# Kernel optimization log

Measured on AMD Instinct MI355X. Metric: run time of the kernel, lower is better.

Reference implementation:

```python
import jax, jax.numpy as jnp
import numpy as np

N, E = 50000, 800000
F_NODE, F_EDGE, H, LAT, MAXN = 128, 16, 128, 64, 200


def setup_inputs() -> dict:
    key = jax.random.key(0)
    ks = jax.random.split(key, 40)
    s = 0.05
    p = {
        'x': jax.random.normal(ks[0], (N, F_NODE), jnp.float32),
        'edge_index': jax.random.randint(ks[1], (2, E), 0, N, jnp.int64),
        'edge_attr': jax.random.normal(ks[2], (E, F_EDGE), jnp.float32),
        'eps': jax.random.normal(ks[3], (1, LAT), jnp.float32),
        'num_nodes': N,
        # GATConv layer 1 (heads=1)
        'W1': jax.random.normal(ks[4], (F_NODE, H), jnp.float32) * s,
        'att_src1': jax.random.normal(ks[5], (H,), jnp.float32) * s,
        'att_dst1': jax.random.normal(ks[6], (H,), jnp.float32) * s,
        'We1': jax.random.normal(ks[7], (F_EDGE, H), jnp.float32) * s,
        'att_e1': jax.random.normal(ks[8], (H,), jnp.float32) * s,
        'b1': jnp.zeros((H,), jnp.float32),
        # GATConv layer 2
        'W2': jax.random.normal(ks[9], (H, H), jnp.float32) * s,
        'att_src2': jax.random.normal(ks[10], (H,), jnp.float32) * s,
        'att_dst2': jax.random.normal(ks[11], (H,), jnp.float32) * s,
        'We2': jax.random.normal(ks[12], (F_EDGE, H), jnp.float32) * s,
        'att_e2': jax.random.normal(ks[13], (H,), jnp.float32) * s,
        'b2': jnp.zeros((H,), jnp.float32),
        # heads
        'mu_W': jax.random.normal(ks[14], (H, LAT), jnp.float32) * s,
        'mu_b': jnp.zeros((LAT,), jnp.float32),
        'lv_W': jax.random.normal(ks[15], (H, LAT), jnp.float32) * s,
        'lv_b': jnp.zeros((LAT,), jnp.float32),
        'dec_W': jax.random.normal(ks[16], (LAT, H), jnp.float32) * s,
        'dec_b': jnp.zeros((H,), jnp.float32),
        'adj_W1': jax.random.normal(ks[17], (H, H), jnp.float32) * s,
        'adj_b1': jnp.zeros((H,), jnp.float32),
        'adj_W2': jax.random.normal(ks[18], (H, MAXN), jnp.float32) * s,
        'adj_b2': jnp.zeros((MAXN,), jnp.float32),
        'nd_W1': jax.random.normal(ks[19], (H, H), jnp.float32) * s,
        'nd_b1': jnp.zeros((H,), jnp.float32),
        'nd_W2': jax.random.normal(ks[20], (H, F_NODE), jnp.float32) * s,
        'nd_b2': jnp.zeros((F_NODE,), jnp.float32),
    }
    return p


def _gat(h, src, dst, ea, W, a_s, a_d, We, a_e, b, n):
    # PyG GATConv, heads=1: linear transform, per-edge attention, segment softmax over dst
    g = h @ W                                     # [n, H]
    alpha = jax.nn.leaky_relu((g @ a_s)[src] + (g @ a_d)[dst] + (ea @ We) @ a_e,
                              negative_slope=0.2)  # [E']
    m = jax.ops.segment_max(alpha, dst, num_segments=n)
    ex = jnp.exp(alpha - m[dst])
    den = jax.ops.segment_sum(ex, dst, num_segments=n)
    w = ex / den[dst]
    return jax.ops.segment_sum(w[:, None] * g[src], dst, num_segments=n) + b


def _forward(x, edge_index, edge_attr, eps, num_nodes,
             W1, att_src1, att_dst1, We1, att_e1, b1,
             W2, att_src2, att_dst2, We2, att_e2, b2,
             mu_W, mu_b, lv_W, lv_b, dec_W, dec_b,
             adj_W1, adj_b1, adj_W2, adj_b2, nd_W1, nd_b1, nd_W2, nd_b2):
    n = x.shape[0]
    src, dst = edge_index[0], edge_index[1]
    # add self loops; self-loop edge_attr = per-node mean of incoming edge_attr (PyG fill_value='mean')
    deg = jax.ops.segment_sum(jnp.ones((src.shape[0],), x.dtype), dst, num_segments=n)
    mean_ea = jax.ops.segment_sum(edge_attr, dst, num_segments=n) / jnp.maximum(deg, 1.0)[:, None]
    loop = jnp.arange(n)
    src_f = jnp.concatenate([src, loop])
    dst_f = jnp.concatenate([dst, loop])
    ea_f = jnp.concatenate([edge_attr, mean_ea])
    h = jax.nn.relu(_gat(x, src_f, dst_f, ea_f, W1, att_src1, att_dst1, We1, att_e1, b1, n))
    h = jax.nn.relu(_gat(h, src_f, dst_f, ea_f, W2, att_src2, att_dst2, We2, att_e2, b2, n))
    hg = h.mean(axis=0, keepdims=True)            # global_mean_pool, single graph -> [1, H]
    mu = hg @ mu_W + mu_b
    logvar = hg @ lv_W + lv_b
    z = mu + eps * jnp.exp(0.5 * logvar)
    hd = jax.nn.relu(z @ dec_W + dec_b)           # [1, H]
    hn = jnp.broadcast_to(hd[:, None, :], (1, num_nodes, hd.shape[-1]))
    adj = jax.nn.relu(hn @ adj_W1 + adj_b1) @ adj_W2 + adj_b2   # [1, n, MAXN]
    adj = adj[:, :, :num_nodes]
    nodes = jax.nn.relu(hn @ nd_W1 + nd_b1) @ nd_W2 + nd_b2     # [1, n, F_NODE]
    return adj, nodes, mu, logvar


def reference(x, edge_index, edge_attr, eps, num_nodes,
              W1, att_src1, att_dst1, We1, att_e1, b1,
              W2, att_src2, att_dst2, We2, att_e2, b2,
              mu_W, mu_b, lv_W, lv_b, dec_W, dec_b,
              adj_W1, adj_b1, adj_W2, adj_b2, nd_W1, nd_b1, nd_W2, nd_b2):
    return _forward(x, edge_index, edge_attr, eps, num_nodes,
                    W1, att_src1, att_dst1, We1, att_e1, b1,
                    W2, att_src2, att_dst2, We2, att_e2, b2,
                    mu_W, mu_b, lv_W, lv_b, dec_W, dec_b,
                    adj_W1, adj_b1, adj_W2, adj_b2, nd_W1, nd_b1, nd_W2, nd_b2)
```

## Files before the change

kernel.cpp:

```cpp
#include <hip/hip_runtime.h>
#include <math.h>

#define NN   50000
#define EE   800000
#define EF   850000
#define HH   128
#define FE   16
#define LATD 64
#define MAXNN 200

#define ADJ_TOT   10000000
#define NODES_TOT 6400000
#define OUT_TOT   16400000
#define MU_OFF    16400000
#define LV_OFF    16400064

typedef __attribute__((ext_vector_type(8))) short bf16x8;
typedef __attribute__((ext_vector_type(4))) float f32x4;
typedef __attribute__((ext_vector_type(2))) float f32x2;

__device__ __forceinline__ unsigned short f2bf(float f){
  unsigned int u = __float_as_uint(f);
  unsigned int r = (u + 0x7FFFu + ((u>>16)&1u)) >> 16;
  return (unsigned short)r;
}
__device__ __forceinline__ float bf2f(unsigned short h){
  return __uint_as_float(((unsigned int)h)<<16);
}

__global__ void ksetup(int* ideg, float* hgsum,
                       const float* We1, const float* ae1, const float* We2, const float* ae2,
                       float* wa1, float* wa2,
                       const float* W1, const float* W2,
                       unsigned short* Wp1, unsigned short* Wp2){
  int i = blockIdx.x*blockDim.x + threadIdx.x;
  if(i < NN) ideg[i]=0;
  if(i < HH) hgsum[i]=0.f;
  if(i < FE){
    float s1=0.f, s2=0.f;
    for(int j=0;j<HH;j++){ s1 += We1[i*HH+j]*ae1[j]; s2 += We2[i*HH+j]*ae2[j]; }
    wa1[i]=s1; wa2[i]=s2;
  }
  if(i < HH*HH){
    int n = i >> 7, k = i & 127;
    Wp1[i] = f2bf(W1[k*HH + n]);
    Wp2[i] = f2bf(W2[k*HH + n]);
  }
}

__global__ void kdeg(const int* __restrict__ ei, int* ideg, unsigned short* __restrict__ erank){
  int e = blockIdx.x*blockDim.x + threadIdx.x;
  if(e<EE) erank[e] = (unsigned short)atomicAdd(&ideg[ei[EE+e]], 1);
}

__global__ void kscan1(const int* __restrict__ ideg, int* rowstart, int* blocksum){
  __shared__ int sd[1024];
  int t=threadIdx.x; int i=blockIdx.x*1024+t;
  int v = (i<NN)? (ideg[i]+1) : 0;
  sd[t]=v; __syncthreads();
  for(int off=1; off<1024; off<<=1){
    int x = (t>=off)? sd[t-off] : 0;
    __syncthreads();
    sd[t] += x;
    __syncthreads();
  }
  if(i<NN) rowstart[i] = sd[t]-v;
  if(t==1023) blocksum[blockIdx.x]=sd[1023];
}
__global__ void kscan2(const int* blocksum, int* blockoff, int nb){
  if(threadIdx.x==0){
    int run=0;
    for(int b=0;b<nb;b++){ blockoff[b]=run; run+=blocksum[b]; }
    blockoff[nb]=run;
  }
}
__global__ void kscan3(int* rowstart, const int* __restrict__ blockoff, int nb){
  int i=blockIdx.x*blockDim.x+threadIdx.x;
  if(i<NN) rowstart[i]+=blockoff[i>>10];
  if(i==0) rowstart[NN]=blockoff[nb];
}

__global__ void kscatter(const int* __restrict__ ei, const float* __restrict__ ea,
                         const float* __restrict__ wa1, const float* __restrict__ wa2,
                         const int* __restrict__ rowstart, const unsigned short* __restrict__ erank,
                         uint2* __restrict__ csr){
  int e=blockIdx.x*blockDim.x+threadIdx.x;
  if(e>=EE) return;
  int s=ei[e], d=ei[EE+e];
  const float4* ea4 = (const float4*)(ea + (size_t)e*FE);
  float4 v0=ea4[0], v1=ea4[1], v2=ea4[2], v3=ea4[3];
  float va[16]={v0.x,v0.y,v0.z,v0.w, v1.x,v1.y,v1.z,v1.w,
                v2.x,v2.y,v2.z,v2.w, v3.x,v3.y,v3.z,v3.w};
  float d1=0.f,d2=0.f;
  #pragma unroll
  for(int f=0;f<FE;f++){ d1+=va[f]*wa1[f]; d2+=va[f]*wa2[f]; }
  int pos = rowstart[d] + (int)erank[e];
  uint2 en; en.x = (unsigned)s;
  en.y = (unsigned)f2bf(d1) | ((unsigned)f2bf(d2)<<16);
  csr[pos] = en;
}

__global__ __launch_bounds__(256) void kself(const int* __restrict__ rowstart,
                      const int* __restrict__ ideg,
                      uint2* __restrict__ csr){
  int tid = threadIdx.x;
  int l16 = tid & 15;
  int grp = tid >> 4;
  int i = blockIdx.x*16 + grp;
  if(i>=NN) return;
  int base = rowstart[i]; int deg = ideg[i];
  float s1=0.f, s2=0.f;
  for(int k=l16;k<deg;k+=16){
    uint2 en=csr[base+k];
    s1 += bf2f((unsigned short)(en.y & 0xFFFFu));
    s2 += bf2f((unsigned short)(en.y >> 16));
  }
  #pragma unroll
  for(int m=8;m>=1;m>>=1){ s1+=__shfl_xor(s1,m,16); s2+=__shfl_xor(s2,m,16); }
  if(l16==0){
    float dg = (float)deg; if(dg<1.f) dg=1.f;
    uint2 en; en.x=(unsigned)i;
    en.y = (unsigned)f2bf(s1/dg) | ((unsigned)f2bf(s2/dg)<<16);
    csr[base+deg] = en;
  }
}

__global__ __launch_bounds__(256) void kgemm3(const void* __restrict__ hin, int h_is_fp32,
    const unsigned short* __restrict__ Wp,
    const float* __restrict__ atts, const float* __restrict__ attd,
    unsigned char* __restrict__ A8, float* __restrict__ asrc, float* __restrict__ adst){
  int lane = threadIdx.x & 63;
  int wid  = threadIdx.x >> 6;
  int l = lane & 15, q = lane >> 4;
  int r0 = blockIdx.x*64 + wid*16;
  if(r0 >= NN) return;
  const unsigned short* hb = (const unsigned short*)hin;
  const float*          hf = (const float*)hin;
  int row = r0 + l;

  f32x4 acc[8];
  #pragma unroll
  for(int t=0;t<8;t++) acc[t]=(f32x4){0.f,0.f,0.f,0.f};

  #pragma unroll
  for(int kb=0;kb<4;kb++){
    bf16x8 a;
    if(h_is_fp32){
      const float* p = hf + (size_t)row*HH + kb*32 + q*8;
      float4 u0 = *(const float4*)(p);
      float4 u1 = *(const float4*)(p+4);
      a[0]=(short)f2bf(u0.x); a[1]=(short)f2bf(u0.y); a[2]=(short)f2bf(u0.z); a[3]=(short)f2bf(u0.w);
      a[4]=(short)f2bf(u1.x); a[5]=(short)f2bf(u1.y); a[6]=(short)f2bf(u1.z); a[7]=(short)f2bf(u1.w);
    } else {
      a = *(const bf16x8*)(hb + (size_t)row*HH + kb*32 + q*8);
    }
    #pragma unroll
    for(int t=0;t<8;t++){
      bf16x8 b = *(const bf16x8*)(Wp + (size_t)(t*16+l)*HH + kb*32 + q*8);
      acc[t] = __builtin_amdgcn_mfma_f32_16x16x32_bf16(a, b, acc[t], 0,0,0);
    }
  }

  float av[8], dv[8];
  #pragma unroll
  for(int t=0;t<8;t++){ av[t]=atts[t*16+l]; dv[t]=attd[t*16+l]; }
  #pragma unroll
  for(int reg=0;reg<4;reg++){
    float ps=0.f, pd=0.f;
    #pragma unroll
    for(int t=0;t<8;t++){ ps+=acc[t][reg]*av[t]; pd+=acc[t][reg]*dv[t]; }
    #pragma unroll
    for(int m=8;m>=1;m>>=1){ ps+=__shfl_xor(ps,m,16); pd+=__shfl_xor(pd,m,16); }
    if(l==0){ int R=r0+q*4+reg; asrc[R]=ps; adst[R]=pd; }
  }
  #pragma unroll
  for(int t=0;t<8;t++)
    #pragma unroll
    for(int reg=0;reg<4;reg++){
      int pk = __builtin_amdgcn_cvt_pk_fp8_f32(acc[t][reg], 0.f, 0, false);
      A8[(size_t)(r0+q*4+reg)*HH + t*16 + l] = (unsigned char)(pk & 0xFF);
    }
}

__global__ __launch_bounds__(256) void kgat(const unsigned char* __restrict__ A8,
    const float* __restrict__ asrc, const float* __restrict__ adst,
    const int* __restrict__ rowstart, const uint2* __restrict__ csr,
    int etsel, const float* __restrict__ bias,
    float* __restrict__ alphabuf, int* __restrict__ srcbuf,
    unsigned short* __restrict__ Bout){
  int lane = threadIdx.x & 63;
  int wid  = threadIdx.x >> 6;
  int i = blockIdx.x*4 + wid;
  if(i >= NN) return;
  int base = rowstart[i]; int len = rowstart[i+1]-base;
  int lq = lane >> 3;
  int lf = lane & 7;
  float adi = adst[i];
  float den;
  float av[16];
  #pragma unroll
  for(int j=0;j<16;j++) av[j]=0.f;

  if(__builtin_expect(len <= 64, 1)){
    float a = -1e30f; int s=0;
    if(lane < len){
      uint2 en = csr[base+lane];
      s = (int)en.x;
      float et = etsel ? bf2f((unsigned short)(en.y>>16)) : bf2f((unsigned short)(en.y&0xFFFFu));
      a = asrc[s] + adi + et;
      a = a>0.f ? a : 0.2f*a;
    }
    float m = a;
    #pragma unroll
    for(int mk=32;mk>=1;mk>>=1) m = fmaxf(m, __shfl_xor(m, mk));
    float ex = (lane<len) ? __expf(a-m) : 0.f;
    float sm = ex;
    #pragma unroll
    for(int mk=32;mk>=1;mk>>=1) sm += __shfl_xor(sm, mk);
    den = sm;
    int chunks = (len+7)>>3;
    float wk = __shfl(ex, lq);
    int   sk = __shfl(s, lq);
    uint4 p  = *((const uint4*)(A8 + (size_t)sk*HH) + lf);
    for(int c=0;c<chunks;c++){
      float wc = wk; uint4 pc = p;
      if(c+1<chunks){
        int idx = (c+1)*8 + lq;
        wk = __shfl(ex, idx);
        sk = __shfl(s, idx);
        p  = *((const uint4*)(A8 + (size_t)sk*HH) + lf);
      }
      f32x2 v;
      v=__builtin_amdgcn_cvt_pk_f32_fp8(pc.x,false); av[0]+=wc*v[0];  av[1]+=wc*v[1];
      v=__builtin_amdgcn_cvt_pk_f32_fp8(pc.x,true ); av[2]+=wc*v[0];  av[3]+=wc*v[1];
      v=__builtin_amdgcn_cvt_pk_f32_fp8(pc.y,false); av[4]+=wc*v[0];  av[5]+=wc*v[1];
      v=__builtin_amdgcn_cvt_pk_f32_fp8(pc.y,true ); av[6]+=wc*v[0];  av[7]+=wc*v[1];
      v=__builtin_amdgcn_cvt_pk_f32_fp8(pc.z,false); av[8]+=wc*v[0];  av[9]+=wc*v[1];
      v=__builtin_amdgcn_cvt_pk_f32_fp8(pc.z,true ); av[10]+=wc*v[0]; av[11]+=wc*v[1];
      v=__builtin_amdgcn_cvt_pk_f32_fp8(pc.w,false); av[12]+=wc*v[0]; av[13]+=wc*v[1];
      v=__builtin_amdgcn_cvt_pk_f32_fp8(pc.w,true ); av[14]+=wc*v[0]; av[15]+=wc*v[1];
    }
  } else {
    float lm = -1e30f;
    for(int k=lane;k<len;k+=64){
      uint2 en = csr[base+k];
      int s = (int)en.x;
      float et = etsel ? bf2f((unsigned short)(en.y>>16)) : bf2f((unsigned short)(en.y&0xFFFFu));
      float a = asrc[s] + adi + et;
      a = a>0.f ? a : 0.2f*a;
      alphabuf[base+k]=a; srcbuf[base+k]=s;
      lm = fmaxf(lm,a);
    }
    #pragma unroll
    for(int mk=32;mk>=1;mk>>=1) lm = fmaxf(lm, __shfl_xor(lm, mk));
    float ls=0.f;
    for(int k=lane;k<len;k+=64){
      float ex = __expf(alphabuf[base+k]-lm);
      alphabuf[base+k]=ex; ls+=ex;
    }
    #pragma unroll
    for(int mk=32;mk>=1;mk>>=1) ls += __shfl_xor(ls, mk);
    den = ls;
    int chunks = (len+7)>>3;
    for(int c=0;c<chunks;c++){
      int idx = c*8 + lq;
      float wc = (idx<len)? alphabuf[base+idx] : 0.f;
      int   sk = (idx<len)? srcbuf[base+idx] : 0;
      uint4 pc = *((const uint4*)(A8 + (size_t)sk*HH) + lf);
      f32x2 v;
      v=__builtin_amdgcn_cvt_pk_f32_fp8(pc.x,false); av[0]+=wc*v[0];  av[1]+=wc*v[1];
      v=__builtin_amdgcn_cvt_pk_f32_fp8(pc.x,true ); av[2]+=wc*v[0];  av[3]+=wc*v[1];
      v=__builtin_amdgcn_cvt_pk_f32_fp8(pc.y,false); av[4]+=wc*v[0];  av[5]+=wc*v[1];
      v=__builtin_amdgcn_cvt_pk_f32_fp8(pc.y,true ); av[6]+=wc*v[0];  av[7]+=wc*v[1];
      v=__builtin_amdgcn_cvt_pk_f32_fp8(pc.z,false); av[8]+=wc*v[0];  av[9]+=wc*v[1];
      v=__builtin_amdgcn_cvt_pk_f32_fp8(pc.z,true ); av[10]+=wc*v[0]; av[11]+=wc*v[1];
      v=__builtin_amdgcn_cvt_pk_f32_fp8(pc.w,false); av[12]+=wc*v[0]; av[13]+=wc*v[1];
      v=__builtin_amdgcn_cvt_pk_f32_fp8(pc.w,true ); av[14]+=wc*v[0]; av[15]+=wc*v[1];
    }
  }
  #pragma unroll
  for(int j=0;j<16;j++){
    av[j] += __shfl_xor(av[j],8);
    av[j] += __shfl_xor(av[j],16);
    av[j] += __shfl_xor(av[j],32);
  }
  if(lq==0){
    float inv = 1.f/den;
    const float4* bp = (const float4*)(bias + lf*16);
    float4 b0=bp[0], b1=bp[1], b2=bp[2], b3=bp[3];
    float o[16];
    o[0] =fmaxf(av[0] *inv+b0.x,0.f); o[1] =fmaxf(av[1] *inv+b0.y,0.f);
    o[2] =fmaxf(av[2] *inv+b0.z,0.f); o[3] =fmaxf(av[3] *inv+b0.w,0.f);
    o[4] =fmaxf(av[4] *inv+b1.x,0.f); o[5] =fmaxf(av[5] *inv+b1.y,0.f);
    o[6] =fmaxf(av[6] *inv+b1.z,0.f); o[7] =fmaxf(av[7] *inv+b1.w,0.f);
    o[8] =fmaxf(av[8] *inv+b2.x,0.f); o[9] =fmaxf(av[9] *inv+b2.y,0.f);
    o[10]=fmaxf(av[10]*inv+b2.z,0.f); o[11]=fmaxf(av[11]*inv+b2.w,0.f);
    o[12]=fmaxf(av[12]*inv+b3.x,0.f); o[13]=fmaxf(av[13]*inv+b3.y,0.f);
    o[14]=fmaxf(av[14]*inv+b3.z,0.f); o[15]=fmaxf(av[15]*inv+b3.w,0.f);
    uint4 ov1, ov2;
    ov1.x=(unsigned)f2bf(o[0]) |((unsigned)f2bf(o[1]) <<16);
    ov1.y=(unsigned)f2bf(o[2]) |((unsigned)f2bf(o[3]) <<16);
    ov1.z=(unsigned)f2bf(o[4]) |((unsigned)f2bf(o[5]) <<16);
    ov1.w=(unsigned)f2bf(o[6]) |((unsigned)f2bf(o[7]) <<16);
    ov2.x=(unsigned)f2bf(o[8]) |((unsigned)f2bf(o[9]) <<16);
    ov2.y=(unsigned)f2bf(o[10])|((unsigned)f2bf(o[11])<<16);
    ov2.z=(unsigned)f2bf(o[12])|((unsigned)f2bf(o[13])<<16);
    ov2.w=(unsigned)f2bf(o[14])|((unsigned)f2bf(o[15])<<16);
    uint4* outp = (uint4*)(Bout + (size_t)i*HH + lf*16);
    outp[0]=ov1; outp[1]=ov2;
  }
}

__global__ __launch_bounds__(256) void khg(const unsigned short* __restrict__ B, float* hgsum){
  int f = threadIdx.x & 127;
  int half = threadIdx.x >> 7;
  float s=0.f;
  for(int i = blockIdx.x*2+half; i < NN; i += gridDim.x*2)
    s += bf2f(B[(size_t)i*HH + f]);
  __shared__ float sd[256];
  sd[threadIdx.x]=s; __syncthreads();
  if(half==0) atomicAdd(&hgsum[f], sd[threadIdx.x]+sd[threadIdx.x+128]);
}

__global__ __launch_bounds__(256) void kdec(const float* __restrict__ hgsum, const float* __restrict__ eps,
   const float* muW,const float* mub,const float* lvW,const float* lvb,
   const float* decW,const float* decb,
   const float* aW1,const float* ab1,const float* aW2,const float* ab2,
   const float* nW1,const float* nb1,const float* nW2,const float* nb2,
   float* out, float* rowadj, float* rownodes){
  __shared__ float hg[HH], z[LATD], hd[HH], t1[HH], t2[HH];
  int t=threadIdx.x;
  if(t<HH) hg[t]=hgsum[t]*(1.0f/NN);
  __syncthreads();
  if(t<LATD){
    float mu=mub[t], lv=lvb[t];
    for(int k=0;k<HH;k++){ mu += hg[k]*muW[k*LATD+t]; lv += hg[k]*lvW[k*LATD+t]; }
    out[MU_OFF+t]=mu; out[LV_OFF+t]=lv;
    z[t]=mu + eps[t]*expf(0.5f*lv);
  }
  __syncthreads();
  if(t<HH){
    float a=decb[t];
    for(int k=0;k<LATD;k++) a += z[k]*decW[k*HH+t];
    hd[t]=fmaxf(a,0.f);
  }
  __syncthreads();
  if(t<HH){
    float a=ab1[t];
    for(int k=0;k<HH;k++) a += hd[k]*aW1[k*HH+t];
    t1[t]=fmaxf(a,0.f);
  } else {
    int j=t-HH;
    float a=nb1[j];
    for(int k=0;k<HH;k++) a += hd[k]*nW1[k*HH+j];
    t2[j]=fmaxf(a,0.f);
  }
  __syncthreads();
  for(int j=t;j<MAXNN;j+=256){
    float a=ab2[j];
    for(int k=0;k<HH;k++) a += t1[k]*aW2[k*MAXNN+j];
    rowadj[j]=a;
  }
  if(t<HH){
    float a=nb2[t];
    for(int k=0;k<HH;k++) a += t2[k]*nW2[k*HH+t];
    rownodes[t]=a;
  }
}

__global__ __launch_bounds__(256) void kbcast(const float* __restrict__ rowadj,
                                              const float* __restrict__ rownodes,
                                              float* __restrict__ out){
  __shared__ float row[MAXNN+HH];
  int t=threadIdx.x;
  if(t<MAXNN) row[t]=rowadj[t];
  if(t<HH) row[MAXNN+t]=rownodes[t];
  __syncthreads();
  int stride=gridDim.x*blockDim.x;
  for(int idx=blockIdx.x*blockDim.x+t; idx<OUT_TOT; idx+=stride){
    if(idx<ADJ_TOT) out[idx]=row[idx%MAXNN];
    else { int j=(idx-ADJ_TOT)&(HH-1); out[idx]=row[MAXNN+j]; }
  }
}

extern "C" void kernel_launch(void* const* d_in, const int* in_sizes, int n_in,
                              void* d_out, int out_size, void* d_ws, size_t ws_size,
                              hipStream_t stream){
  const float* x   = (const float*)d_in[0];
  const int*   ei  = (const int*)d_in[1];
  const float* ea  = (const float*)d_in[2];
  const float* eps = (const float*)d_in[3];
  const float* W1  =(const float*)d_in[5];
  const float* as1 =(const float*)d_in[6];
  const float* ad1 =(const float*)d_in[7];
  const float* We1 =(const float*)d_in[8];
  const float* ae1 =(const float*)d_in[9];
  const float* b1  =(const float*)d_in[10];
  const float* W2  =(const float*)d_in[11];
  const float* as2 =(const float*)d_in[12];
  const float* ad2 =(const float*)d_in[13];
  const float* We2 =(const float*)d_in[14];
  const float* ae2 =(const float*)d_in[15];
  const float* b2  =(const float*)d_in[16];
  const float* muW =(const float*)d_in[17];
  const float* mub =(const float*)d_in[18];
  const float* lvW =(const float*)d_in[19];
  const float* lvb =(const float*)d_in[20];
  const float* decW=(const float*)d_in[21];
  const float* decb=(const float*)d_in[22];
  const float* aW1 =(const float*)d_in[23];
  const float* ab1 =(const float*)d_in[24];
  const float* aW2 =(const float*)d_in[25];
  const float* ab2 =(const float*)d_in[26];
  const float* nW1 =(const float*)d_in[27];
  const float* nb1 =(const float*)d_in[28];
  const float* nW2 =(const float*)d_in[29];
  const float* nb2 =(const float*)d_in[30];
  float* out=(float*)d_out;

  char* w=(char*)d_ws;
  unsigned char*  A8  = (unsigned char*)w;  w += (size_t)NN*HH;
  unsigned short* Bbf = (unsigned short*)w; w += (size_t)NN*HH*2;
  unsigned short* Wp1 = (unsigned short*)w; w += (size_t)HH*HH*2;
  unsigned short* Wp2 = (unsigned short*)w; w += (size_t)HH*HH*2;
  uint2*  csr      = (uint2*)w;  w += (size_t)EF*8;
  float*  alphabuf = (float*)w;  w += (size_t)EF*4;
  int*    srcbuf   = (int*)w;    w += (size_t)EF*4;
  unsigned short* erank = (unsigned short*)w; w += (size_t)EE*2;
  int*    rowstart = (int*)w;    w += (size_t)(NN+1)*4;
  int*    ideg     = (int*)w;    w += (size_t)NN*4;
  float*  asrc     = (float*)w;  w += (size_t)NN*4;
  float*  adst     = (float*)w;  w += (size_t)NN*4;
  float*  hgsum    = (float*)w;  w += 128*4;
  float*  wa1      = (float*)w;  w += 16*4;
  float*  wa2      = (float*)w;  w += 16*4;
  float*  rowadj   = (float*)w;  w += 256*4;
  float*  rownodes = (float*)w;  w += 128*4;
  int*    blocksum = (int*)w;    w += 64*4;
  int*    blockoff = (int*)w;    w += 64*4;

  int nb = (NN+1023)/1024;
  int gemmblocks = (NN+63)/64;
  int gatblocks  = (NN+3)/4;

  hipLaunchKernelGGL(ksetup, dim3((NN+255)/256), dim3(256), 0, stream,
                     ideg, hgsum, We1, ae1, We2, ae2, wa1, wa2, W1, W2, Wp1, Wp2);
  hipLaunchKernelGGL(kdeg, dim3((EE+255)/256), dim3(256), 0, stream, ei, ideg, erank);
  hipLaunchKernelGGL(kscan1, dim3(nb), dim3(1024), 0, stream, ideg, rowstart, blocksum);
  hipLaunchKernelGGL(kscan2, dim3(1), dim3(64), 0, stream, blocksum, blockoff, nb);
  hipLaunchKernelGGL(kscan3, dim3((NN+255)/256), dim3(256), 0, stream, rowstart, blockoff, nb);
  hipLaunchKernelGGL(kscatter, dim3((EE+255)/256), dim3(256), 0, stream,
                     ei, ea, wa1, wa2, rowstart, erank, csr);
  hipLaunchKernelGGL(kself, dim3((NN+15)/16), dim3(256), 0, stream, rowstart, ideg, csr);
  hipLaunchKernelGGL(kgemm3, dim3(gemmblocks), dim3(256), 0, stream,
                     (const void*)x, 1, Wp1, as1, ad1, A8, asrc, adst);
  hipLaunchKernelGGL(kgat,  dim3(gatblocks), dim3(256), 0, stream, A8, asrc, adst, rowstart, csr, 0, b1, alphabuf, srcbuf, Bbf);
  hipLaunchKernelGGL(kgemm3, dim3(gemmblocks), dim3(256), 0, stream,
                     (const void*)Bbf, 0, Wp2, as2, ad2, A8, asrc, adst);
  hipLaunchKernelGGL(kgat,  dim3(gatblocks), dim3(256), 0, stream, A8, asrc, adst, rowstart, csr, 1, b2, alphabuf, srcbuf, Bbf);
  hipLaunchKernelGGL(khg,   dim3(512), dim3(256), 0, stream, Bbf, hgsum);
  hipLaunchKernelGGL(kdec,  dim3(1), dim3(256), 0, stream, hgsum, eps,
                     muW,mub,lvW,lvb,decW,decb,aW1,ab1,aW2,ab2,nW1,nb1,nW2,nb2,
                     out, rowadj, rownodes);
  hipLaunchKernelGGL(kbcast, dim3(2048), dim3(256), 0, stream, rowadj, rownodes, out);
}
```

Baseline: 441.3 us.

## Fuse setup/degree and scatter/gemm kernels, fold self-loop into GAT, vectorize broadcast

Merges the degree-count kernel with setup, replaces the zeroing with a memset, and runs scatter and the first GEMM as disjoint block ranges of one launch. The separate self-loop kernel is removed; the GAT kernel now computes the mean edge-attention of the self loop itself. The aggregation switches from 8-lane chunked uint4 loads to a per-neighbor readlane loop, with each lane handling two features and normalising up front. The single-thread kscan2 becomes a wave shuffle scan, and the broadcast writes float4. The aim is fewer launches and less work per node, at the cost of more serial per-neighbor loads in the GAT loop.

```diff
diff --git a/kernel.cpp b/kernel.cpp
--- a/kernel.cpp
+++ b/kernel.cpp
@@ -15,6 +15,9 @@
 #define MU_OFF    16400000
 #define LV_OFF    16400064
 
+#define SCATBLOCKS 3125
+#define GEMMBLOCKS 782
+
 typedef __attribute__((ext_vector_type(8))) short bf16x8;
 typedef __attribute__((ext_vector_type(4))) float f32x4;
 typedef __attribute__((ext_vector_type(2))) float f32x2;
@@ -27,15 +30,18 @@
 __device__ __forceinline__ float bf2f(unsigned short h){
   return __uint_as_float(((unsigned int)h)<<16);
 }
-
-__global__ void ksetup(int* ideg, float* hgsum,
+__device__ __forceinline__ float rlanef(float v, int k){
+  return __int_as_float(__builtin_amdgcn_readlane(__float_as_int(v), k));
+}
+
+__global__ __launch_bounds__(256) void kdegsetup(const int* __restrict__ ei, int* ideg,
+                       unsigned short* __restrict__ erank,
                        const float* We1, const float* ae1, const float* We2, const float* ae2,
                        float* wa1, float* wa2,
                        const float* W1, const float* W2,
                        unsigned short* Wp1, unsigned short* Wp2){
-  int i = blockIdx.x*blockDim.x + threadIdx.x;
-  if(i < NN) ideg[i]=0;
-  if(i < HH) hgsum[i]=0.f;
+  int i = blockIdx.x*256 + threadIdx.x;
+  if(i < EE) erank[i] = (unsigned short)atomicAdd(&ideg[ei[EE+i]], 1);
   if(i < FE){
     float s1=0.f, s2=0.f;
     for(int j=0;j<HH;j++){ s1 += We1[i*HH+j]*ae1[j]; s2 += We2[i*HH+j]*ae2[j]; }
@@ -46,11 +52,6 @@
     Wp1[i] = f2bf(W1[k*HH + n]);
     Wp2[i] = f2bf(W2[k*HH + n]);
   }
-}
-
-__global__ void kdeg(const int* __restrict__ ei, int* ideg, unsigned short* __restrict__ erank){
-  int e = blockIdx.x*blockDim.x + threadIdx.x;
-  if(e<EE) erank[e] = (unsigned short)atomicAdd(&ideg[ei[EE+e]], 1);
 }
 
 __global__ void kscan1(const int* __restrict__ ideg, int* rowstart, int* blocksum){
@@ -67,12 +68,16 @@
   if(i<NN) rowstart[i] = sd[t]-v;
   if(t==1023) blocksum[blockIdx.x]=sd[1023];
 }
-__global__ void kscan2(const int* blocksum, int* blockoff, int nb){
-  if(threadIdx.x==0){
-    int run=0;
-    for(int b=0;b<nb;b++){ blockoff[b]=run; run+=blocksum[b]; }
-    blockoff[nb]=run;
-  }
+__global__ void kscan2(const int* __restrict__ blocksum, int* __restrict__ blockoff, int nb){
+  int t = threadIdx.x;
+  int v = (t<nb)? blocksum[t] : 0;
+  int inc = v;
+  #pragma unroll
+  for(int off=1; off<64; off<<=1){
+    int x = __shfl_up(inc, off);
+    if(t>=off) inc += x;
+  }
+  if(t<=nb) blockoff[t] = inc - v;
 }
 __global__ void kscan3(int* rowstart, const int* __restrict__ blockoff, int nb){
   int i=blockIdx.x*blockDim.x+threadIdx.x;
@@ -80,11 +85,11 @@
   if(i==0) rowstart[NN]=blockoff[nb];
 }
 
-__global__ void kscatter(const int* __restrict__ ei, const float* __restrict__ ea,
+__device__ __forceinline__ void scatter_body(int e,
+                         const int* __restrict__ ei, const float* __restrict__ ea,
                          const float* __restrict__ wa1, const float* __restrict__ wa2,
                          const int* __restrict__ rowstart, const unsigned short* __restrict__ erank,
                          uint2* __restrict__ csr){
-  int e=blockIdx.x*blockDim.x+threadIdx.x;
   if(e>=EE) return;
   int s=ei[e], d=ei[EE+e];
   const float4* ea4 = (const float4*)(ea + (size_t)e*FE);
@@ -100,39 +105,14 @@
   csr[pos] = en;
 }
 
-__global__ __launch_bounds__(256) void kself(const int* __restrict__ rowstart,
-                      const int* __restrict__ ideg,
-                      uint2* __restrict__ csr){
-  int tid = threadIdx.x;
-  int l16 = tid & 15;
-  int grp = tid >> 4;
-  int i = blockIdx.x*16 + grp;
-  if(i>=NN) return;
-  int base = rowstart[i]; int deg = ideg[i];
-  float s1=0.f, s2=0.f;
-  for(int k=l16;k<deg;k+=16){
-    uint2 en=csr[base+k];
-    s1 += bf2f((unsigned short)(en.y & 0xFFFFu));
-    s2 += bf2f((unsigned short)(en.y >> 16));
-  }
-  #pragma unroll
-  for(int m=8;m>=1;m>>=1){ s1+=__shfl_xor(s1,m,16); s2+=__shfl_xor(s2,m,16); }
-  if(l16==0){
-    float dg = (float)deg; if(dg<1.f) dg=1.f;
-    uint2 en; en.x=(unsigned)i;
-    en.y = (unsigned)f2bf(s1/dg) | ((unsigned)f2bf(s2/dg)<<16);
-    csr[base+deg] = en;
-  }
-}
-
-__global__ __launch_bounds__(256) void kgemm3(const void* __restrict__ hin, int h_is_fp32,
+__device__ __forceinline__ void gemm_body(int bid, int tid, const void* __restrict__ hin, int h_is_fp32,
     const unsigned short* __restrict__ Wp,
     const float* __restrict__ atts, const float* __restrict__ attd,
     unsigned char* __restrict__ A8, float* __restrict__ asrc, float* __restrict__ adst){
-  int lane = threadIdx.x & 63;
-  int wid  = threadIdx.x >> 6;
+  int lane = tid & 63;
+  int wid  = tid >> 6;
   int l = lane & 15, q = lane >> 4;
-  int r0 = blockIdx.x*64 + wid*16;
+  int r0 = bid*64 + wid*16;
   if(r0 >= NN) return;
   const unsigned short* hb = (const unsigned short*)hin;
   const float*          hf = (const float*)hin;
@@ -182,6 +162,29 @@
     }
 }
 
+__global__ __launch_bounds__(256) void kgemm3(const void* __restrict__ hin, int h_is_fp32,
+    const unsigned short* __restrict__ Wp,
+    const float* __restrict__ atts, const float* __restrict__ attd,
+    unsigned char* __restrict__ A8, float* __restrict__ asrc, float* __restrict__ adst){
+  gemm_body(blockIdx.x, threadIdx.x, hin, h_is_fp32, Wp, atts, attd, A8, asrc, adst);
+}
+
+__global__ __launch_bounds__(256) void kscatgemm(
+    const int* __restrict__ ei, const float* __restrict__ ea,
+    const float* __restrict__ wa1, const float* __restrict__ wa2,
+    const int* __restrict__ rowstart, const unsigned short* __restrict__ erank,
+    uint2* __restrict__ csr,
+    const void* __restrict__ hin, int h_is_fp32,
+    const unsigned short* __restrict__ Wp,
+    const float* __restrict__ atts, const float* __restrict__ attd,
+    unsigned char* __restrict__ A8, float* __restrict__ asrc, float* __restrict__ adst){
+  if(blockIdx.x < SCATBLOCKS){
+    scatter_body(blockIdx.x*256 + threadIdx.x, ei, ea, wa1, wa2, rowstart, erank, csr);
+  } else {
+    gemm_body(blockIdx.x - SCATBLOCKS, threadIdx.x, hin, h_is_fp32, Wp, atts, attd, A8, asrc, adst);
+  }
+}
+
 __global__ __launch_bounds__(256) void kgat(const unsigned char* __restrict__ A8,
     const float* __restrict__ asrc, const float* __restrict__ adst,
     const int* __restrict__ rowstart, const uint2* __restrict__ csr,
@@ -192,123 +195,99 @@
   int wid  = threadIdx.x >> 6;
   int i = blockIdx.x*4 + wid;
   if(i >= NN) return;
-  int base = rowstart[i]; int len = rowstart[i+1]-base;
-  int lq = lane >> 3;
-  int lf = lane & 7;
+  int base = rowstart[i];
+  int len  = rowstart[i+1]-base;
   float adi = adst[i];
-  float den;
-  float av[16];
-  #pragma unroll
-  for(int j=0;j<16;j++) av[j]=0.f;
+  float a0=0.f, a1=0.f;
 
   if(__builtin_expect(len <= 64, 1)){
-    float a = -1e30f; int s=0;
-    if(lane < len){
+    int s = i; float et = 0.f;
+    if(lane < len-1){
       uint2 en = csr[base+lane];
       s = (int)en.x;
-      float et = etsel ? bf2f((unsigned short)(en.y>>16)) : bf2f((unsigned short)(en.y&0xFFFFu));
+      et = etsel ? bf2f((unsigned short)(en.y>>16)) : bf2f((unsigned short)(en.y & 0xFFFFu));
+    }
+    float ets = (lane < len-1) ? et : 0.f;
+    #pragma unroll
+    for(int mk=32;mk>=1;mk>>=1) ets += __shfl_xor(ets,mk);
+    if(lane == len-1) et = ets / fmaxf((float)(len-1), 1.f);
+    float a = -1e30f;
+    if(lane < len){
       a = asrc[s] + adi + et;
-      a = a>0.f ? a : 0.2f*a;
+      a = fmaxf(a, 0.2f*a);
     }
     float m = a;
     #pragma unroll
-    for(int mk=32;mk>=1;mk>>=1) m = fmaxf(m, __shfl_xor(m, mk));
+    for(int mk=32;mk>=1;mk>>=1) m = fmaxf(m, __shfl_xor(m,mk));
     float ex = (lane<len) ? __expf(a-m) : 0.f;
     float sm = ex;
     #pragma unroll
-    for(int mk=32;mk>=1;mk>>=1) sm += __shfl_xor(sm, mk);
-    den = sm;
-    int chunks = (len+7)>>3;
-    float wk = __shfl(ex, lq);
-    int   sk = __shfl(s, lq);
-    uint4 p  = *((const uint4*)(A8 + (size_t)sk*HH) + lf);
-    for(int c=0;c<chunks;c++){
-      float wc = wk; uint4 pc = p;
-      if(c+1<chunks){
-        int idx = (c+1)*8 + lq;
-        wk = __shfl(ex, idx);
-        sk = __shfl(s, idx);
-        p  = *((const uint4*)(A8 + (size_t)sk*HH) + lf);
-      }
-      f32x2 v;
-      v=__builtin_amdgcn_cvt_pk_f32_fp8(pc.x,false); av[0]+=wc*v[0];  av[1]+=wc*v[1];
-      v=__builtin_amdgcn_cvt_pk_f32_fp8(pc.x,true ); av[2]+=wc*v[0];  av[3]+=wc*v[1];
-      v=__builtin_amdgcn_cvt_pk_f32_fp8(pc.y,false); av[4]+=wc*v[0];  av[5]+=wc*v[1];
-      v=__builtin_amdgcn_cvt_pk_f32_fp8(pc.y,true ); av[6]+=wc*v[0];  av[7]+=wc*v[1];
-      v=__builtin_amdgcn_cvt_pk_f32_fp8(pc.z,false); av[8]+=wc*v[0];  av[9]+=wc*v[1];
-      v=__builtin_amdgcn_cvt_pk_f32_fp8(pc.z,true ); av[10]+=wc*v[0]; av[11]+=wc*v[1];
-      v=__builtin_amdgcn_cvt_pk_f32_fp8(pc.w,false); av[12]+=wc*v[0]; av[13]+=wc*v[1];
-      v=__builtin_amdgcn_cvt_pk_f32_fp8(pc.w,true ); av[14]+=wc*v[0]; av[15]+=wc*v[1];
+    for(int mk=32;mk>=1;mk>>=1) sm += __shfl_xor(sm,mk);
+    ex *= __builtin_amdgcn_rcpf(sm);
+
+    #pragma unroll 4
+    for(int k=0;k<len;k++){
+      int   sk = __builtin_amdgcn_readlane(s, k);
+      float wk = rlanef(ex, k);
+      unsigned u = *(const unsigned short*)(A8 + (size_t)sk*HH + lane*2);
+      f32x2 v = __builtin_amdgcn_cvt_pk_f32_fp8((int)u, false);
+      a0 += wk*v[0]; a1 += wk*v[1];
     }
   } else {
-    float lm = -1e30f;
-    for(int k=lane;k<len;k+=64){
+    int deg = len-1;
+    float lm = -1e30f, ets = 0.f;
+    for(int k=lane;k<deg;k+=64){
       uint2 en = csr[base+k];
-      int s = (int)en.x;
-      float et = etsel ? bf2f((unsigned short)(en.y>>16)) : bf2f((unsigned short)(en.y&0xFFFFu));
-      float a = asrc[s] + adi + et;
-      a = a>0.f ? a : 0.2f*a;
-      alphabuf[base+k]=a; srcbuf[base+k]=s;
+      int sr = (int)en.x;
+      float et = etsel ? bf2f((unsigned short)(en.y>>16)) : bf2f((unsigned short)(en.y & 0xFFFFu));
+      ets += et;
+      float a = asrc[sr] + adi + et;
+      a = fmaxf(a, 0.2f*a);
+      alphabuf[base+k]=a; srcbuf[base+k]=sr;
       lm = fmaxf(lm,a);
     }
     #pragma unroll
-    for(int mk=32;mk>=1;mk>>=1) lm = fmaxf(lm, __shfl_xor(lm, mk));
+    for(int mk=32;mk>=1;mk>>=1){
+      ets += __shfl_xor(ets,mk);
+      lm   = fmaxf(lm, __shfl_xor(lm,mk));
+    }
+    float aself = asrc[i] + adi + ets/(float)deg;
+    aself = fmaxf(aself, 0.2f*aself);
+    lm = fmaxf(lm, aself);
     float ls=0.f;
     for(int k=lane;k<len;k+=64){
-      float ex = __expf(alphabuf[base+k]-lm);
-      alphabuf[base+k]=ex; ls+=ex;
-    }
-    #pragma unroll
-    for(int mk=32;mk>=1;mk>>=1) ls += __shfl_xor(ls, mk);
-    den = ls;
-    int chunks = (len+7)>>3;
-    for(int c=0;c<chunks;c++){
-      int idx = c*8 + lq;
-      float wc = (idx<len)? alphabuf[base+idx] : 0.f;
-      int   sk = (idx<len)? srcbuf[base+idx] : 0;
-      uint4 pc = *((const uint4*)(A8 + (size_t)sk*HH) + lf);
-      f32x2 v;
-      v=__builtin_amdgcn_cvt_pk_f32_fp8(pc.x,false); av[0]+=wc*v[0];  av[1]+=wc*v[1];
-      v=__builtin_amdgcn_cvt_pk_f32_fp8(pc.x,true ); av[2]+=wc*v[0];  av[3]+=wc*v[1];
-      v=__builtin_amdgcn_cvt_pk_f32_fp8(pc.y,false); av[4]+=wc*v[0];  av[5]+=wc*v[1];
-      v=__builtin_amdgcn_cvt_pk_f32_fp8(pc.y,true ); av[6]+=wc*v[0];  av[7]+=wc*v[1];
-      v=__builtin_amdgcn_cvt_pk_f32_fp8(pc.z,false); av[8]+=wc*v[0];  av[9]+=wc*v[1];
-      v=__builtin_amdgcn_cvt_pk_f32_fp8(pc.z,true ); av[10]+=wc*v[0]; av[11]+=wc*v[1];
-      v=__builtin_amdgcn_cvt_pk_f32_fp8(pc.w,false); av[12]+=wc*v[0]; av[13]+=wc*v[1];
-      v=__builtin_amdgcn_cvt_pk_f32_fp8(pc.w,true ); av[14]+=wc*v[0]; av[15]+=wc*v[1];
-    }
-  }
-  #pragma unroll
-  for(int j=0;j<16;j++){
-    av[j] += __shfl_xor(av[j],8);
-    av[j] += __shfl_xor(av[j],16);
-    av[j] += __shfl_xor(av[j],32);
-  }
-  if(lq==0){
-    float inv = 1.f/den;
-    const float4* bp = (const float4*)(bias + lf*16);
-    float4 b0=bp[0], b1=bp[1], b2=bp[2], b3=bp[3];
-    float o[16];
-    o[0] =fmaxf(av[0] *inv+b0.x,0.f); o[1] =fmaxf(av[1] *inv+b0.y,0.f);
-    o[2] =fmaxf(av[2] *inv+b0.z,0.f); o[3] =fmaxf(av[3] *inv+b0.w,0.f);
-    o[4] =fmaxf(av[4] *inv+b1.x,0.f); o[5] =fmaxf(av[5] *inv+b1.y,0.f);
-    o[6] =fmaxf(av[6] *inv+b1.z,0.f); o[7] =fmaxf(av[7] *inv+b1.w,0.f);
-    o[8] =fmaxf(av[8] *inv+b2.x,0.f); o[9] =fmaxf(av[9] *inv+b2.y,0.f);
-    o[10]=fmaxf(av[10]*inv+b2.z,0.f); o[11]=fmaxf(av[11]*inv+b2.w,0.f);
-    o[12]=fmaxf(av[12]*inv+b3.x,0.f); o[13]=fmaxf(av[13]*inv+b3.y,0.f);
-    o[14]=fmaxf(av[14]*inv+b3.z,0.f); o[15]=fmaxf(av[15]*inv+b3.w,0.f);
-    uint4 ov1, ov2;
-    ov1.x=(unsigned)f2bf(o[0]) |((unsigned)f2bf(o[1]) <<16);
-    ov1.y=(unsigned)f2bf(o[2]) |((unsigned)f2bf(o[3]) <<16);
-    ov1.z=(unsigned)f2bf(o[4]) |((unsigned)f2bf(o[5]) <<16);
-    ov1.w=(unsigned)f2bf(o[6]) |((unsigned)f2bf(o[7]) <<16);
-    ov2.x=(unsigned)f2bf(o[8]) |((unsigned)f2bf(o[9]) <<16);
-    ov2.y=(unsigned)f2bf(o[10])|((unsigned)f2bf(o[11])<<16);
-    ov2.z=(unsigned)f2bf(o[12])|((unsigned)f2bf(o[13])<<16);
-    ov2.w=(unsigned)f2bf(o[14])|((unsigned)f2bf(o[15])<<16);
-    uint4* outp = (uint4*)(Bout + (size_t)i*HH + lf*16);
-    outp[0]=ov1; outp[1]=ov2;
-  }
+      float a = (k<deg)? alphabuf[base+k] : aself;
+      float e_ = __expf(a-lm);
+      alphabuf[base+k]=e_;
+      ls += e_;
+    }
+    #pragma unroll
+    for(int mk=32;mk>=1;mk>>=1) ls += __shfl_xor(ls,mk);
+    float inv = 1.f/ls;
+    for(int k0=0;k0<len;k0+=64){
+      int kk = k0+lane;
+      int sv = 0; float ev = 0.f;
+      if(kk<len){
+        sv = (kk<deg)? srcbuf[base+kk] : i;
+        ev = alphabuf[base+kk]*inv;
+      }
+      int nmax = len-k0; if(nmax>64) nmax=64;
+      #pragma unroll 4
+      for(int j=0;j<nmax;j++){
+        int   sk = __builtin_amdgcn_readlane(sv, j);
+        float wk = rlanef(ev, j);
+        unsigned u = *(const unsigned short*)(A8 + (size_t)sk*HH + lane*2);
+        f32x2 v = __builtin_amdgcn_cvt_pk_f32_fp8((int)u, false);
+        a0 += wk*v[0]; a1 += wk*v[1];
+      }
+    }
+  }
+
+  float2 bv = *(const float2*)(bias + lane*2);
+  float o0 = fmaxf(a0 + bv.x, 0.f);
+  float o1 = fmaxf(a1 + bv.y, 0.f);
+  unsigned pk = (unsigned)f2bf(o0) | ((unsigned)f2bf(o1)<<16);
+  *(unsigned*)(Bout + (size_t)i*HH + lane*2) = pk;
 }
 
 __global__ __launch_bounds__(256) void khg(const unsigned short* __restrict__ B, float* hgsum){
@@ -334,6 +313,7 @@
   __syncthreads();
   if(t<LATD){
     float mu=mub[t], lv=lvb[t];
+    #pragma unroll 8
     for(int k=0;k<HH;k++){ mu += hg[k]*muW[k*LATD+t]; lv += hg[k]*lvW[k*LATD+t]; }
     out[MU_OFF+t]=mu; out[LV_OFF+t]=lv;
     z[t]=mu + eps[t]*expf(0.5f*lv);
@@ -341,28 +321,33 @@
   __syncthreads();
   if(t<HH){
     float a=decb[t];
+    #pragma unroll 8
     for(int k=0;k<LATD;k++) a += z[k]*decW[k*HH+t];
     hd[t]=fmaxf(a,0.f);
   }
   __syncthreads();
   if(t<HH){
     float a=ab1[t];
+    #pragma unroll 8
     for(int k=0;k<HH;k++) a += hd[k]*aW1[k*HH+t];
     t1[t]=fmaxf(a,0.f);
   } else {
     int j=t-HH;
     float a=nb1[j];
+    #pragma unroll 8
     for(int k=0;k<HH;k++) a += hd[k]*nW1[k*HH+j];
     t2[j]=fmaxf(a,0.f);
   }
   __syncthreads();
   for(int j=t;j<MAXNN;j+=256){
     float a=ab2[j];
+    #pragma unroll 8
     for(int k=0;k<HH;k++) a += t1[k]*aW2[k*MAXNN+j];
     rowadj[j]=a;
   }
   if(t<HH){
     float a=nb2[t];
+    #pragma unroll 8
     for(int k=0;k<HH;k++) a += t2[k]*nW2[k*HH+t];
     rownodes[t]=a;
   }
@@ -377,9 +362,18 @@
   if(t<HH) row[MAXNN+t]=rownodes[t];
   __syncthreads();
   int stride=gridDim.x*blockDim.x;
-  for(int idx=blockIdx.x*blockDim.x+t; idx<OUT_TOT; idx+=stride){
-    if(idx<ADJ_TOT) out[idx]=row[idx%MAXNN];
-    else { int j=(idx-ADJ_TOT)&(HH-1); out[idx]=row[MAXNN+j]; }
+  const int tot4 = OUT_TOT/4;
+  for(int q=blockIdx.x*blockDim.x+t; q<tot4; q+=stride){
+    int idx = q*4;
+    float4 vv;
+    if(idx<ADJ_TOT){
+      int j = idx % MAXNN;
+      vv = *(const float4*)&row[j];
+    } else {
+      int j = (idx-ADJ_TOT) & (HH-1);
+      vv = *(const float4*)&row[MAXNN+j];
+    }
+    *(float4*)&out[idx] = vv;
   }
 }
 
@@ -429,9 +423,9 @@
   unsigned short* erank = (unsigned short*)w; w += (size_t)EE*2;
   int*    rowstart = (int*)w;    w += (size_t)(NN+1)*4;
   int*    ideg     = (int*)w;    w += (size_t)NN*4;
+  float*  hgsum    = (float*)w;  w += 128*4;
   float*  asrc     = (float*)w;  w += (size_t)NN*4;
   float*  adst     = (float*)w;  w += (size_t)NN*4;
-  float*  hgsum    = (float*)w;  w += 128*4;
   float*  wa1      = (float*)w;  w += 16*4;
   float*  wa2      = (float*)w;  w += 16*4;
   float*  rowadj   = (float*)w;  w += 256*4;
@@ -440,24 +434,23 @@
   int*    blockoff = (int*)w;    w += 64*4;
 
   int nb = (NN+1023)/1024;
-  int gemmblocks = (NN+63)/64;
   int gatblocks  = (NN+3)/4;
 
-  hipLaunchKernelGGL(ksetup, dim3((NN+255)/256), dim3(256), 0, stream,
-                     ideg, hgsum, We1, ae1, We2, ae2, wa1, wa2, W1, W2, Wp1, Wp2);
-  hipLaunchKernelGGL(kdeg, dim3((EE+255)/256), dim3(256), 0, stream, ei, ideg, erank);
+  hipMemsetAsync(ideg, 0, (size_t)(NN+128)*4, stream);
+  hipLaunchKernelGGL(kdegsetup, dim3((EE+255)/256), dim3(256), 0, stream,
+                     ei, ideg, erank, We1, ae1, We2, ae2, wa1, wa2, W1, W2, Wp1, Wp2);
   hipLaunchKernelGGL(kscan1, dim3(nb), dim3(1024), 0, stream, ideg, rowstart, blocksum);
   hipLaunchKernelGGL(kscan2, dim3(1), dim3(64), 0, stream, blocksum, blockoff, nb);
   hipLaunchKernelGGL(kscan3, dim3((NN+255)/256), dim3(256), 0, stream, rowstart, blockoff, nb);
-  hipLaunchKernelGGL(kscatter, dim3((EE+255)/256), dim3(256), 0, stream,
-                     ei, ea, wa1, wa2, rowstart, erank, csr);
-  hipLaunchKernelGGL(kself, dim3((NN+15)/16), dim3(256), 0, stream, rowstart, ideg, csr);
-  hipLaunchKernelGGL(kgemm3, dim3(gemmblocks), dim3(256), 0, stream,
+  hipLaunchKernelGGL(kscatgemm, dim3(SCATBLOCKS+GEMMBLOCKS), dim3(256), 0, stream,
+                     ei, ea, wa1, wa2, rowstart, erank, csr,
                      (const void*)x, 1, Wp1, as1, ad1, A8, asrc, adst);
-  hipLaunchKernelGGL(kgat,  dim3(gatblocks), dim3(256), 0, stream, A8, asrc, adst, rowstart, csr, 0, b1, alphabuf, srcbuf, Bbf);
-  hipLaunchKernelGGL(kgemm3, dim3(gemmblocks), dim3(256), 0, stream,
+  hipLaunchKernelGGL(kgat,  dim3(gatblocks), dim3(256), 0, stream,
+                     A8, asrc, adst, rowstart, csr, 0, b1, alphabuf, srcbuf, Bbf);
+  hipLaunchKernelGGL(kgemm3, dim3(GEMMBLOCKS), dim3(256), 0, stream,
                      (const void*)Bbf, 0, Wp2, as2, ad2, A8, asrc, adst);
-  hipLaunchKernelGGL(kgat,  dim3(gatblocks), dim3(256), 0, stream, A8, asrc, adst, rowstart, csr, 1, b2, alphabuf, srcbuf, Bbf);
+  hipLaunchKernelGGL(kgat,  dim3(gatblocks), dim3(256), 0, stream,
+                     A8, asrc, adst, rowstart, csr, 1, b2, alphabuf, srcbuf, Bbf);
   hipLaunchKernelGGL(khg,   dim3(512), dim3(256), 0, stream, Bbf, hgsum);
   hipLaunchKernelGGL(kdec,  dim3(1), dim3(256), 0, stream, hgsum, eps,
                      muW,mub,lvW,lvb,decW,decb,aW1,ab1,aW2,ab2,nW1,nb1,nW2,nb2,
```

Measured after the change: 465.5 us. +5.5%, slower.
